# Optimization experiments

Hardware: AMD Instinct MI355X
Metric: run time of the kernel (lower is better)

## Reference

```python
import jax, jax.numpy as jnp
import numpy as np
from jax import lax

# module constants (from init_kwargs)
IN_CH = 128
OUT_CH = 128
CTX = 128
KS = 3
STRIDE = 1
PAD = 1
GROUPS = 1
ATT_GROUPS = 1
K = 4
TEMP = 30.0  # T_max, used as the fixed temperature at init


def setup_inputs() -> dict:
    key = jax.random.key(0)
    k1, k2, k3, k4, k5 = jax.random.split(key, 5)
    b, f, t = 16, 64, 256
    x = jax.random.normal(k1, (b, IN_CH, f, t), dtype=jnp.float32)
    g = jax.random.normal(k2, (1, b, CTX), dtype=jnp.float32)
    # Dense(k*att_groups) params (kaiming-normal kernel, zero bias)
    fan_in = CTX
    dense_kernel = jax.random.normal(k3, (CTX, K * ATT_GROUPS), dtype=jnp.float32) * np.sqrt(2.0 / fan_in)
    dense_bias = jnp.zeros((K * ATT_GROUPS,), dtype=jnp.float32)
    # kernel bank: (k, out, in//groups, ks, ks) -> swapaxes(1,2) -> flatten to (1, att_groups, k, -1)
    flat = OUT_CH * (IN_CH // GROUPS) * KS * KS // ATT_GROUPS
    weight = jax.random.normal(k4, (1, ATT_GROUPS, K, flat), dtype=jnp.float32) * np.sqrt(2.0 / flat)
    return {"x": x, "g": g, "dense_kernel": dense_kernel, "dense_bias": dense_bias, "weight": weight}


def reference(x, g, dense_kernel, dense_bias, weight):
    b, c, f, t = x.shape
    g_c = g[0].reshape(b, -1)                                  # [b, ctx]
    residuals = (g_c @ dense_kernel + dense_bias).reshape(b, ATT_GROUPS, 1, -1)  # [b, ag, 1, k]
    attention = jax.nn.softmax(residuals / TEMP, axis=-1)      # [b, ag, 1, k]
    # per-sample kernel aggregation: [b, ag, 1, k] @ [1, ag, k, D] -> [b, ag, 1, D]
    agg = (attention @ weight).swapaxes(1, 2)                  # [b, 1, ag, D]
    agg = agg.reshape(b * OUT_CH, IN_CH // GROUPS, KS, KS)
    # batch-as-groups grouped conv
    out = lax.conv_general_dilated(
        x.reshape(1, b * c, f, t), agg,
        window_strides=(STRIDE, STRIDE),
        padding=[(PAD, PAD), (PAD, PAD)],
        dimension_numbers=("NCHW", "OIHW", "NCHW"),
        feature_group_count=b * GROUPS,
    )
    return out.reshape(b, OUT_CH, out.shape[-2], out.shape[-1])
```

## Files before the change

### kernel.cpp

```cpp
#include <hip/hip_runtime.h>
#include <stdint.h>

#define NB 16
#define NC 128
#define NOC 128
#define NF 64
#define NT 256
#define NCTX 128
#define NTAPS 9
#define NFLAT 147456
#define TEMPR 30.0f

#define SXCOLS 130
#define SX_CH (3*4*SXCOLS)

typedef float f32x4 __attribute__((ext_vector_type(4)));
typedef __bf16 bf16x8 __attribute__((ext_vector_type(8)));

__global__ void attn_kernel(const float* __restrict__ g,
                            const float* __restrict__ dk,
                            const float* __restrict__ bias,
                            float* __restrict__ att) {
    int b = threadIdx.x;
    if (b >= NB) return;
    float r0 = bias[0], r1 = bias[1], r2 = bias[2], r3 = bias[3];
    const float* gb = g + b * NCTX;
    for (int c = 0; c < NCTX; ++c) {
        float gv = gb[c];
        r0 += gv * dk[c*4+0];
        r1 += gv * dk[c*4+1];
        r2 += gv * dk[c*4+2];
        r3 += gv * dk[c*4+3];
    }
    r0 *= (1.0f/TEMPR); r1 *= (1.0f/TEMPR); r2 *= (1.0f/TEMPR); r3 *= (1.0f/TEMPR);
    float mx = fmaxf(fmaxf(r0, r1), fmaxf(r2, r3));
    float e0 = expf(r0-mx), e1 = expf(r1-mx), e2 = expf(r2-mx), e3 = expf(r3-mx);
    float s = e0+e1+e2+e3;
    att[b*4+0] = e0/s; att[b*4+1] = e1/s; att[b*4+2] = e2/s; att[b*4+3] = e3/s;
}

__global__ void agg_kernel(const float* __restrict__ w,
                           const float* __restrict__ att,
                           unsigned short* __restrict__ wb) {
    int idx = blockIdx.x * 256 + threadIdx.x;
    int ic = idx & 127;
    int oc = (idx >> 7) & 127;
    int b  = idx >> 14;
    float a0 = att[b*4+0], a1 = att[b*4+1], a2 = att[b*4+2], a3 = att[b*4+3];
    int d0 = (oc*NC + ic) * NTAPS;
    int c4 = ic >> 5;
    int kq = (ic >> 3) & 3;
    int e  = ic & 7;
    #pragma unroll
    for (int tap = 0; tap < NTAPS; ++tap) {
        float s = a0 * w[0*NFLAT + d0 + tap]
                + a1 * w[1*NFLAT + d0 + tap]
                + a2 * w[2*NFLAT + d0 + tap]
                + a3 * w[3*NFLAT + d0 + tap];
        __bf16 h = (__bf16)s;
        unsigned short u = *(unsigned short*)&h;
        int chunk = (tap * 4 + kq) * 128 + oc;
        wb[(((b * 4 + c4) * (NTAPS*4*NOC)) + chunk) * 8 + e] = u;
    }
}

__global__ __launch_bounds__(256) void conv_kernel(
        const float* __restrict__ x,
        const unsigned short* __restrict__ wb,
        float* __restrict__ out) {
    __shared__ __align__(16) unsigned short sx[SX_CH * 8];

    const int p_  = blockIdx.x;
    const int lg  = (p_ & 7) * 256 + (p_ >> 3);
    const int b   = lg >> 7;
    const int y   = (lg >> 1) & 63;
    const int t0  = (lg & 1) * 128;

    const int tid  = threadIdx.x;
    const int lane = tid & 63;
    const int wid  = tid >> 6;
    const int wpix = wid & 1;
    const int woc  = wid >> 1;
    const int l15  = lane & 15;
    const int l4   = lane >> 4;

    f32x4 acc[4][4];
    #pragma unroll
    for (int m = 0; m < 4; ++m)
        #pragma unroll
        for (int n = 0; n < 4; ++n)
            acc[m][n] = (f32x4){0.f, 0.f, 0.f, 0.f};

    const float* xb = x + (b * NC) * (NF * NT);
    const unsigned short* wbb = wb + b * (4 * NTAPS * 4 * NOC) * 8;

    const unsigned short* const wfrag = wbb + (l4 * 128 + woc * 64 + l15) * 8;

    const unsigned short* const sxp = sx + (l4 * SXCOLS + wpix * 64 + l15) * 8;

    for (int c4 = 0; c4 < 4; ++c4) {
        const int ic0 = c4 * 32;
        const unsigned short* const wc4 = wfrag + (c4 * NTAPS * 4 * NOC) * 8;

        bf16x8 afc0 = *(const bf16x8*)(wc4 + (0 * 16) * 8);
        bf16x8 afc1 = *(const bf16x8*)(wc4 + (1 * 16) * 8);
        bf16x8 afc2 = *(const bf16x8*)(wc4 + (2 * 16) * 8);
        bf16x8 afc3 = *(const bf16x8*)(wc4 + (3 * 16) * 8);

        __syncthreads();

        #pragma unroll
        for (int j = 0; j < 6; ++j) {
            const int u  = tid + j * 256;
            const int e  = u & 3;
            const int kq = (u >> 2) & 3;
            const int q  = (u >> 4) & 31;
            const int r  = u >> 9;
            const int iy = y - 1 + r;
            const int ic = ic0 + kq * 8 + e * 2;
            f32x4 v0 = (f32x4){0.f,0.f,0.f,0.f};
            f32x4 v1 = v0;
            if ((unsigned)iy < (unsigned)NF) {
                const float* src = xb + (ic * NF + iy) * NT + t0 + q * 4;
                v0 = *(const f32x4*)src;
                v1 = *(const f32x4*)(src + NF * NT);
            }
            unsigned short* dst = sx + ((r * 4 + kq) * SXCOLS + q * 4 + 1) * 8 + e * 2;
            #pragma unroll
            for (int jj = 0; jj < 4; ++jj) {
                __bf16 h0 = (__bf16)v0[jj];
                __bf16 h1 = (__bf16)v1[jj];
                unsigned pk = (unsigned)*(unsigned short*)&h0
                            | ((unsigned)*(unsigned short*)&h1 << 16);
                *(unsigned*)(dst + jj * 8) = pk;
            }
        }
        if (tid < 96) {
            const int e    = tid & 3;
            const int kq   = (tid >> 2) & 3;
            const int side = (tid >> 4) & 1;
            const int r    = tid >> 5;
            const int c    = side ? (SXCOLS - 1) : 0;
            const int t    = t0 - 1 + c;
            const int iy   = y - 1 + r;
            const int ic   = ic0 + kq * 8 + e * 2;
            float f0 = 0.f, f1 = 0.f;
            if ((unsigned)iy < (unsigned)NF && (unsigned)t < (unsigned)NT) {
                const float* src = xb + (ic * NF + iy) * NT + t;
                f0 = src[0];
                f1 = src[NF * NT];
            }
            __bf16 h0 = (__bf16)f0;
            __bf16 h1 = (__bf16)f1;
            unsigned pk = (unsigned)*(unsigned short*)&h0
                        | ((unsigned)*(unsigned short*)&h1 << 16);
            *(unsigned*)(sx + ((r * 4 + kq) * SXCOLS + c) * 8 + e * 2) = pk;
        }
        __syncthreads();

        #pragma unroll
        for (int tap = 0; tap < 9; ++tap) {
            const int ky = tap / 3;
            const int kx = tap % 3;
            bf16x8 afn0, afn1, afn2, afn3;
            if (tap < 8) {
                const unsigned short* wt = wc4 + ((tap + 1) * 4 * NOC) * 8;
                afn0 = *(const bf16x8*)(wt + (0 * 16) * 8);
                afn1 = *(const bf16x8*)(wt + (1 * 16) * 8);
                afn2 = *(const bf16x8*)(wt + (2 * 16) * 8);
                afn3 = *(const bf16x8*)(wt + (3 * 16) * 8);
            }
            bf16x8 bfv[4];
            #pragma unroll
            for (int n = 0; n < 4; ++n)
                bfv[n] = *(const bf16x8*)(sxp + (ky * 4 * SXCOLS + n * 16 + kx) * 8);
            #pragma unroll
            for (int n = 0; n < 4; ++n) {
                acc[0][n] = __builtin_amdgcn_mfma_f32_16x16x32_bf16(afc0, bfv[n], acc[0][n], 0, 0, 0);
                acc[1][n] = __builtin_amdgcn_mfma_f32_16x16x32_bf16(afc1, bfv[n], acc[1][n], 0, 0, 0);
                acc[2][n] = __builtin_amdgcn_mfma_f32_16x16x32_bf16(afc2, bfv[n], acc[2][n], 0, 0, 0);
                acc[3][n] = __builtin_amdgcn_mfma_f32_16x16x32_bf16(afc3, bfv[n], acc[3][n], 0, 0, 0);
            }
            if (tap < 8) { afc0 = afn0; afc1 = afn1; afc2 = afn2; afc3 = afn3; }
        }
    }

    #pragma unroll
    for (int m = 0; m < 4; ++m) {
        int ocb = woc * 64 + m * 16 + l4 * 4;
        #pragma unroll
        for (int r = 0; r < 4; ++r) {
            float* orow = out + ((b * NOC + ocb + r) * NF + y) * NT + t0;
            #pragma unroll
            for (int n = 0; n < 4; ++n)
                orow[wpix * 64 + n * 16 + l15] = acc[m][n][r];
        }
    }
}

extern "C" void kernel_launch(void* const* d_in, const int* in_sizes, int n_in,
                              void* d_out, int out_size, void* d_ws, size_t ws_size,
                              hipStream_t stream) {
    const float* x    = (const float*)d_in[0];
    const float* g    = (const float*)d_in[1];
    const float* dk   = (const float*)d_in[2];
    const float* bias = (const float*)d_in[3];
    const float* w    = (const float*)d_in[4];
    float* out = (float*)d_out;

    float* att = (float*)d_ws;
    unsigned short* wb = (unsigned short*)((char*)d_ws + 256);

    attn_kernel<<<dim3(1), dim3(64), 0, stream>>>(g, dk, bias, att);
    agg_kernel<<<dim3(1024), dim3(256), 0, stream>>>(w, att, wb);
    conv_kernel<<<dim3(2048), dim3(256), 0, stream>>>(x, wb, out);
}
```

Before: 129.4 us.

## Prefetch next channel chunk into registers, deepen weight prefetch, swizzle LDS columns

```diff
diff --git a/kernel.cpp b/kernel.cpp
--- a/kernel.cpp
+++ b/kernel.cpp
@@ -93,31 +93,29 @@
 
     const float* xb = x + (b * NC) * (NF * NT);
     const unsigned short* wbb = wb + b * (4 * NTAPS * 4 * NOC) * 8;
-
-    const unsigned short* const wfrag = wbb + (l4 * 128 + woc * 64 + l15) * 8;
-
-    const unsigned short* const sxp = sx + (l4 * SXCOLS + wpix * 64 + l15) * 8;
-
-    for (int c4 = 0; c4 < 4; ++c4) {
-        const int ic0 = c4 * 32;
-        const unsigned short* const wc4 = wfrag + (c4 * NTAPS * 4 * NOC) * 8;
-
-        bf16x8 afc0 = *(const bf16x8*)(wc4 + (0 * 16) * 8);
-        bf16x8 afc1 = *(const bf16x8*)(wc4 + (1 * 16) * 8);
-        bf16x8 afc2 = *(const bf16x8*)(wc4 + (2 * 16) * 8);
-        bf16x8 afc3 = *(const bf16x8*)(wc4 + (3 * 16) * 8);
-
-        __syncthreads();
-
+    const int wlane = (l4 * 128 + woc * 64 + l15) * 8;
+
+    const int se  = tid & 3;
+    const int skq = (tid >> 2) & 3;
+    const int sd  = skq >> 1;
+
+    const int rd  = l4 >> 1;
+    int cb0 = (wpix * 64 + l15 + 0) ^ rd;
+    int cb1 = (wpix * 64 + l15 + 1) ^ rd;
+    int cb2 = (wpix * 64 + l15 + 2) ^ rd;
+
+    f32x4 xv0[6], xv1[6];
+    float bf0 = 0.f, bf1 = 0.f;
+    bf16x8 ar0[4], ar1[4], ar2[4];
+
+    auto issue_x = [&](int c4) {
+        const int ic = c4 * 32 + skq * 8 + se * 2;
         #pragma unroll
         for (int j = 0; j < 6; ++j) {
-            const int u  = tid + j * 256;
-            const int e  = u & 3;
-            const int kq = (u >> 2) & 3;
-            const int q  = (u >> 4) & 31;
-            const int r  = u >> 9;
+            const int u = tid + j * 256;
+            const int q = (u >> 4) & 31;
+            const int r = u >> 9;
             const int iy = y - 1 + r;
-            const int ic = ic0 + kq * 8 + e * 2;
             f32x4 v0 = (f32x4){0.f,0.f,0.f,0.f};
             f32x4 v1 = v0;
             if ((unsigned)iy < (unsigned)NF) {
@@ -125,63 +123,102 @@
                 v0 = *(const f32x4*)src;
                 v1 = *(const f32x4*)(src + NF * NT);
             }
-            unsigned short* dst = sx + ((r * 4 + kq) * SXCOLS + q * 4 + 1) * 8 + e * 2;
-            #pragma unroll
-            for (int jj = 0; jj < 4; ++jj) {
-                __bf16 h0 = (__bf16)v0[jj];
-                __bf16 h1 = (__bf16)v1[jj];
-                unsigned pk = (unsigned)*(unsigned short*)&h0
-                            | ((unsigned)*(unsigned short*)&h1 << 16);
-                *(unsigned*)(dst + jj * 8) = pk;
-            }
-        }
+            xv0[j] = v0;
+            xv1[j] = v1;
+        }
+        bf0 = 0.f; bf1 = 0.f;
         if (tid < 96) {
             const int e    = tid & 3;
             const int kq   = (tid >> 2) & 3;
             const int side = (tid >> 4) & 1;
             const int r    = tid >> 5;
-            const int c    = side ? (SXCOLS - 1) : 0;
-            const int t    = t0 - 1 + c;
+            const int t    = side ? (t0 + 128) : (t0 - 1);
             const int iy   = y - 1 + r;
-            const int ic   = ic0 + kq * 8 + e * 2;
-            float f0 = 0.f, f1 = 0.f;
+            const int ic   = c4 * 32 + kq * 8 + e * 2;
             if ((unsigned)iy < (unsigned)NF && (unsigned)t < (unsigned)NT) {
                 const float* src = xb + (ic * NF + iy) * NT + t;
-                f0 = src[0];
-                f1 = src[NF * NT];
-            }
-            __bf16 h0 = (__bf16)f0;
-            __bf16 h1 = (__bf16)f1;
+                bf0 = src[0];
+                bf1 = src[NF * NT];
+            }
+        }
+    };
+
+    auto write_x = [&]() {
+        #pragma unroll
+        for (int j = 0; j < 6; ++j) {
+            const int u = tid + j * 256;
+            const int q = (u >> 4) & 31;
+            const int r = u >> 9;
+            unsigned short* base = sx + ((r * 4 + skq) * SXCOLS) * 8 + se * 2;
+            #pragma unroll
+            for (int jj = 0; jj < 4; ++jj) {
+                const int colp = (q * 4 + 1 + jj) ^ sd;
+                __bf16 h0 = (__bf16)xv0[j][jj];
+                __bf16 h1 = (__bf16)xv1[j][jj];
+                unsigned pk = (unsigned)*(unsigned short*)&h0
+                            | ((unsigned)*(unsigned short*)&h1 << 16);
+                *(unsigned*)(base + colp * 8) = pk;
+            }
+        }
+        if (tid < 96) {
+            const int e    = tid & 3;
+            const int kq   = (tid >> 2) & 3;
+            const int side = (tid >> 4) & 1;
+            const int r    = tid >> 5;
+            const int colp = (side ? (SXCOLS - 1) : 0) ^ (kq >> 1);
+            __bf16 h0 = (__bf16)bf0;
+            __bf16 h1 = (__bf16)bf1;
             unsigned pk = (unsigned)*(unsigned short*)&h0
                         | ((unsigned)*(unsigned short*)&h1 << 16);
-            *(unsigned*)(sx + ((r * 4 + kq) * SXCOLS + c) * 8 + e * 2) = pk;
-        }
-        __syncthreads();
+            *(unsigned*)(sx + ((r * 4 + kq) * SXCOLS + colp) * 8 + e * 2) = pk;
+        }
+    };
+
+    auto loadA = [&](bf16x8* dst, int c4, int tap) {
+        const unsigned short* wt = wbb + ((c4 * NTAPS + tap) * 4 * NOC) * 8 + wlane;
+        dst[0] = *(const bf16x8*)(wt);
+        dst[1] = *(const bf16x8*)(wt + 16 * 8);
+        dst[2] = *(const bf16x8*)(wt + 32 * 8);
+        dst[3] = *(const bf16x8*)(wt + 48 * 8);
+    };
+
+    issue_x(0);
+    loadA(ar0, 0, 0);
+    loadA(ar1, 0, 1);
+    loadA(ar2, 0, 2);
+    write_x();
+    __syncthreads();
+
+    for (int c4 = 0; c4 < 4; ++c4) {
+        if (c4 < 3) issue_x(c4 + 1);
 
         #pragma unroll
         for (int tap = 0; tap < 9; ++tap) {
+            bf16x8* cur = (tap % 3 == 0) ? ar0 : (tap % 3 == 1) ? ar1 : ar2;
             const int ky = tap / 3;
             const int kx = tap % 3;
-            bf16x8 afn0, afn1, afn2, afn3;
-            if (tap < 8) {
-                const unsigned short* wt = wc4 + ((tap + 1) * 4 * NOC) * 8;
-                afn0 = *(const bf16x8*)(wt + (0 * 16) * 8);
-                afn1 = *(const bf16x8*)(wt + (1 * 16) * 8);
-                afn2 = *(const bf16x8*)(wt + (2 * 16) * 8);
-                afn3 = *(const bf16x8*)(wt + (3 * 16) * 8);
-            }
+            const int cbk = (kx == 0) ? cb0 : (kx == 1) ? cb1 : cb2;
             bf16x8 bfv[4];
             #pragma unroll
             for (int n = 0; n < 4; ++n)
-                bfv[n] = *(const bf16x8*)(sxp + (ky * 4 * SXCOLS + n * 16 + kx) * 8);
+                bfv[n] = *(const bf16x8*)(sx + (((ky * 4 + l4) * SXCOLS) + cbk + n * 16) * 8);
             #pragma unroll
             for (int n = 0; n < 4; ++n) {
-                acc[0][n] = __builtin_amdgcn_mfma_f32_16x16x32_bf16(afc0, bfv[n], acc[0][n], 0, 0, 0);
-                acc[1][n] = __builtin_amdgcn_mfma_f32_16x16x32_bf16(afc1, bfv[n], acc[1][n], 0, 0, 0);
-                acc[2][n] = __builtin_amdgcn_mfma_f32_16x16x32_bf16(afc2, bfv[n], acc[2][n], 0, 0, 0);
-                acc[3][n] = __builtin_amdgcn_mfma_f32_16x16x32_bf16(afc3, bfv[n], acc[3][n], 0, 0, 0);
-            }
-            if (tap < 8) { afc0 = afn0; afc1 = afn1; afc2 = afn2; afc3 = afn3; }
+                acc[0][n] = __builtin_amdgcn_mfma_f32_16x16x32_bf16(cur[0], bfv[n], acc[0][n], 0, 0, 0);
+                acc[1][n] = __builtin_amdgcn_mfma_f32_16x16x32_bf16(cur[1], bfv[n], acc[1][n], 0, 0, 0);
+                acc[2][n] = __builtin_amdgcn_mfma_f32_16x16x32_bf16(cur[2], bfv[n], acc[2][n], 0, 0, 0);
+                acc[3][n] = __builtin_amdgcn_mfma_f32_16x16x32_bf16(cur[3], bfv[n], acc[3][n], 0, 0, 0);
+            }
+            if (tap < 6) loadA(cur, c4, tap + 3);
+        }
+
+        if (c4 < 3) {
+            loadA(ar0, c4 + 1, 0);
+            loadA(ar1, c4 + 1, 1);
+            loadA(ar2, c4 + 1, 2);
+            __syncthreads();
+            write_x();
+            __syncthreads();
         }
     }
 
```

Result: slower. 190.1 us (+46.9%).
